# Optimization experiments

Measured on AMD Instinct MI355X. Metric: run time of the kernel, lower is better.

## Reference

```python
import jax, jax.numpy as jnp
import numpy as np

N = 50000   # total nodes
E = 600000  # total edges
D = 128     # feature dim (node_dim == all gcn_dims)
G = 128     # graphs in batch
LN_EPS = 1e-5


def setup_inputs() -> dict:
    key = jax.random.key(0)
    ks = jax.random.split(key, 16)
    inp = {
        "x": jax.random.normal(ks[0], (N, D), dtype=jnp.float32),
        "edge_index": jax.random.randint(ks[1], (2, E), 0, N),
        "batch": jnp.sort(jax.random.randint(ks[2], (N,), 0, G)),
    }
    for l in range(3):
        inp[f"W{l}"] = jax.random.normal(ks[3 + 4 * l], (D, D), dtype=jnp.float32) / np.float32(np.sqrt(D))
        inp[f"b{l}"] = jnp.zeros((D,), jnp.float32)
        inp[f"g{l}"] = jnp.ones((D,), jnp.float32)   # LayerNorm weight
        inp[f"be{l}"] = jnp.zeros((D,), jnp.float32)  # LayerNorm bias
    return inp


def _gcn_norm(edge_index):
    # PyG GCNConv default: add self-loops, symmetric deg^-1/2 normalization.
    loop = jnp.arange(N, dtype=edge_index.dtype)
    src = jnp.concatenate([edge_index[0], loop])
    dst = jnp.concatenate([edge_index[1], loop])
    deg = jax.ops.segment_sum(jnp.ones(src.shape[0], jnp.float32), dst, num_segments=N)
    dinv = jnp.where(deg > 0, jax.lax.rsqrt(deg), 0.0)
    norm = dinv[src] * dinv[dst]  # [E+N]
    return src, dst, norm


def _block(x, src, dst, norm, W, b, g, be):
    # GCNConv: gather-transform-scatter
    h = x @ W                                   # [N, D]
    msg = h[src] * norm[:, None]                # [E+N, D] gather + scale
    out = jax.ops.segment_sum(msg, dst, num_segments=N) + b
    # LayerNorm
    mu = jnp.mean(out, axis=-1, keepdims=True)
    var = jnp.mean((out - mu) ** 2, axis=-1, keepdims=True)
    out = (out - mu) * jax.lax.rsqrt(var + LN_EPS) * g + be
    # residual (Identity since in==out channels) + SiLU
    return jax.nn.silu(out + x)


def reference(x, edge_index, batch, W0, b0, g0, be0, W1, b1, g1, be1, W2, b2, g2, be2):
    src, dst, norm = _gcn_norm(edge_index)
    params = [(W0, b0, g0, be0), (W1, b1, g1, be1), (W2, b2, g2, be2)]
    for (W, b, g, be) in params:
        x = _block(x, src, dst, norm, W, b, g, be)
    # global mean pool over batch ids
    counts = jax.ops.segment_sum(jnp.ones((N,), jnp.float32), batch, num_segments=G)
    sums = jax.ops.segment_sum(x, batch, num_segments=G)
    return sums / jnp.maximum(counts, 1.0)[:, None]
```

## Files before the change

### kernel.cpp

```cpp
#include <hip/hip_runtime.h>
#include <math.h>

#define DD 128

typedef __attribute__((ext_vector_type(8))) short short8;
typedef __attribute__((ext_vector_type(4))) float f32x4;

__device__ __forceinline__ unsigned short f2b(float f) {
    unsigned int x = __float_as_uint(f);
    return (unsigned short)((x + 0x7FFFu + ((x >> 16) & 1u)) >> 16);
}
__device__ __forceinline__ float b2f(unsigned short u) {
    return __uint_as_float(((unsigned int)u) << 16);
}

__global__ __launch_bounds__(256) void k_count(const int* __restrict__ dst, int* __restrict__ cnt, int E) {
    int e = blockIdx.x * 256 + threadIdx.x;
    if (e < E) atomicAdd(&cnt[dst[e]], 1);
}

__global__ __launch_bounds__(256) void k_scan1(const int* __restrict__ cnt, int* __restrict__ part, int N) {
    __shared__ int lds[256];
    int t = threadIdx.x;
    int i = blockIdx.x * 256 + t;
    lds[t] = (i < N) ? cnt[i] : 0;
    __syncthreads();
#pragma unroll
    for (int off = 128; off > 0; off >>= 1) {
        if (t < off) lds[t] += lds[t + off];
        __syncthreads();
    }
    if (t == 0) part[blockIdx.x] = lds[0];
}

__global__ __launch_bounds__(1024) void k_scan2(int* __restrict__ part, int* __restrict__ rowptr,
                                                int nblk, int N) {
    __shared__ int lds[1024];
    int t = threadIdx.x;
    int v = (t < nblk) ? part[t] : 0;
    lds[t] = v;
    __syncthreads();
    for (int off = 1; off < 1024; off <<= 1) {
        int u = (t >= off) ? lds[t - off] : 0;
        __syncthreads();
        lds[t] += u;
        __syncthreads();
    }
    if (t < nblk) part[t] = lds[t] - v;
    if (t == 1023) rowptr[N] = lds[1023];
}

__global__ __launch_bounds__(256) void k_scan3(const int* __restrict__ cnt, const int* __restrict__ part,
                                               int* __restrict__ rowptr, float* __restrict__ dinv, int N) {
    __shared__ int lds[256];
    int t = threadIdx.x;
    int i = blockIdx.x * 256 + t;
    int v = (i < N) ? cnt[i] : 0;
    lds[t] = v;
    __syncthreads();
    for (int off = 1; off < 256; off <<= 1) {
        int u = (t >= off) ? lds[t - off] : 0;
        __syncthreads();
        lds[t] += u;
        __syncthreads();
    }
    if (i < N) {
        rowptr[i] = part[blockIdx.x] + lds[t] - v;
        dinv[i] = rsqrtf((float)v + 1.0f);
    }
}

__global__ __launch_bounds__(256) void k_fill(const int* __restrict__ src, const int* __restrict__ dst,
                                              const float* __restrict__ dinv, const int* __restrict__ rowptr,
                                              int* __restrict__ cursor, int2* __restrict__ adj, int E) {
    int e = blockIdx.x * 256 + threadIdx.x;
    if (e >= E) return;
    int s = src[e], d = dst[e];
    int pos = atomicAdd(&cursor[d], 1);
    float w = dinv[s] * dinv[d];
    adj[rowptr[d] + pos] = make_int2(s, __float_as_int(w));
}

__global__ __launch_bounds__(256) void k_prepW3(const float* __restrict__ W0, const float* __restrict__ W1,
                                                const float* __restrict__ W2, unsigned short* __restrict__ T0,
                                                unsigned short* __restrict__ T1, unsigned short* __restrict__ T2) {
    int l = blockIdx.x >> 6;
    const float* W = (l == 0) ? W0 : (l == 1) ? W1 : W2;
    unsigned short* WT = (l == 0) ? T0 : (l == 1) ? T1 : T2;
    int idx = (blockIdx.x & 63) * 256 + threadIdx.x;
    int k = idx >> 7, c = idx & 127;
    WT[c * DD + k] = f2b(W[idx]);
}

template <int IN_BF16>
__global__ __launch_bounds__(256) void k_gemm_mfma(const void* __restrict__ Xv,
                                                   const unsigned short* __restrict__ WT,
                                                   unsigned short* __restrict__ H, int N) {
    __shared__ __align__(16) unsigned short sB[DD * DD];
    __shared__ __align__(16) unsigned short sA[64 * DD];
    int tid = threadIdx.x;
    long row0 = (long)blockIdx.x * 64;

#pragma unroll
    for (int i = 0; i < 8; ++i) {
        int q = tid + 256 * i;
        int c = q >> 4, j = q & 15;
        short8 v = *(const short8*)(WT + q * 8);
        int byte = c * 256 + ((j * 16) ^ ((c & 7) << 4));
        *(short8*)((char*)sB + byte) = v;
    }
#pragma unroll
    for (int i = 0; i < 4; ++i) {
        int q = tid + 256 * i;
        int r = q >> 4, j = q & 15;
        short8 v;
        if (IN_BF16) {
#pragma unroll
            for (int z = 0; z < 8; ++z) v[z] = 0;
            if (row0 + r < N) v = *(const short8*)((const unsigned short*)Xv + (row0 + r) * DD + j * 8);
        } else {
            float4 a0 = make_float4(0.f, 0.f, 0.f, 0.f), a1 = a0;
            if (row0 + r < N) {
                const float4* p = (const float4*)((const float*)Xv + (row0 + r) * DD + j * 8);
                a0 = p[0];
                a1 = p[1];
            }
            v[0] = (short)f2b(a0.x); v[1] = (short)f2b(a0.y);
            v[2] = (short)f2b(a0.z); v[3] = (short)f2b(a0.w);
            v[4] = (short)f2b(a1.x); v[5] = (short)f2b(a1.y);
            v[6] = (short)f2b(a1.z); v[7] = (short)f2b(a1.w);
        }
        int byte = r * 256 + ((j * 16) ^ ((r & 7) << 4));
        *(short8*)((char*)sA + byte) = v;
    }
    __syncthreads();

    int w = tid >> 6, l = tid & 63;
    int lr = l & 15, kg = l >> 4;
    f32x4 acc[8] = {};

#pragma unroll
    for (int step = 0; step < 4; ++step) {
        int ar = w * 16 + lr;
        int abyte = ar * 256 + ((step * 64 + kg * 16) ^ ((ar & 7) << 4));
        short8 af = *(const short8*)((const char*)sA + abyte);
#pragma unroll
        for (int ct = 0; ct < 8; ++ct) {
            int c = ct * 16 + lr;
            int bbyte = c * 256 + ((step * 64 + kg * 16) ^ ((c & 7) << 4));
            short8 bf = *(const short8*)((const char*)sB + bbyte);
            acc[ct] = __builtin_amdgcn_mfma_f32_16x16x32_bf16(af, bf, acc[ct], 0, 0, 0);
        }
    }

#pragma unroll
    for (int ct = 0; ct < 8; ++ct) {
#pragma unroll
        for (int reg = 0; reg < 4; ++reg) {
            long r = row0 + w * 16 + kg * 4 + reg;
            if (r < N) H[r * DD + ct * 16 + lr] = f2b(acc[ct][reg]);
        }
    }
}

template <int IN_BF16>
__global__ __launch_bounds__(256) void k_agg(const unsigned short* __restrict__ h, const void* __restrict__ xin,
                                             const int* __restrict__ rowptr, const int2* __restrict__ adj,
                                             const float* __restrict__ dinv, const float* __restrict__ b,
                                             const float* __restrict__ g, const float* __restrict__ be,
                                             unsigned int* __restrict__ xout, int N) {
    int row = blockIdx.x * 4 + (threadIdx.x >> 6);
    if (row >= N) return;
    int lane = threadIdx.x & 63;
    const unsigned int* hu = (const unsigned int*)h;

    float dv = dinv[row];
    float dv2 = dv * dv;
    unsigned int us = hu[(size_t)row * 64 + lane];
    float2 bv = ((const float2*)b)[lane];
    float2 acc = make_float2(fmaf(b2f((unsigned short)(us & 0xFFFF)), dv2, bv.x),
                             fmaf(b2f((unsigned short)(us >> 16)), dv2, bv.y));

    int beg = rowptr[row], end = rowptr[row + 1];
    for (int j0 = beg; j0 < end; j0 += 64) {
        int myj = j0 + lane;
        int2 a = make_int2(0, 0);
        if (myj < end) a = adj[myj];
        int cnt = min(64, end - j0);
        int cntR = (cnt + 7) & ~7;
        for (int k0 = 0; k0 < cntR; k0 += 8) {
            unsigned int un[8];
            float wt[8];
#pragma unroll
            for (int u = 0; u < 8; ++u) {
                int s = __shfl(a.x, k0 + u, 64);
                wt[u] = __int_as_float(__shfl(a.y, k0 + u, 64));
                un[u] = hu[(size_t)s * 64 + lane];
            }
#pragma unroll
            for (int u = 0; u < 8; ++u) {
                acc.x = fmaf(wt[u], b2f((unsigned short)(un[u] & 0xFFFF)), acc.x);
                acc.y = fmaf(wt[u], b2f((unsigned short)(un[u] >> 16)), acc.y);
            }
        }
    }

    float ssum = acc.x + acc.y;
#pragma unroll
    for (int o = 32; o > 0; o >>= 1) ssum += __shfl_xor(ssum, o, 64);
    float mu = ssum * (1.0f / 128.0f);
    float dx0 = acc.x - mu, dx1 = acc.y - mu;
    float vs = dx0 * dx0 + dx1 * dx1;
#pragma unroll
    for (int o = 32; o > 0; o >>= 1) vs += __shfl_xor(vs, o, 64);
    float rstd = rsqrtf(vs * (1.0f / 128.0f) + 1e-5f);

    float2 gv = ((const float2*)g)[lane];
    float2 bev = ((const float2*)be)[lane];
    float2 xv;
    if (IN_BF16) {
        unsigned int xu = ((const unsigned int*)xin)[(size_t)row * 64 + lane];
        xv = make_float2(b2f((unsigned short)(xu & 0xFFFF)), b2f((unsigned short)(xu >> 16)));
    } else {
        xv = ((const float2*)xin)[(size_t)row * 64 + lane];
    }
    float a0 = fmaf(dx0 * rstd, gv.x, bev.x) + xv.x;
    float a1 = fmaf(dx1 * rstd, gv.y, bev.y) + xv.y;
    a0 = a0 / (1.0f + expf(-a0));
    a1 = a1 / (1.0f + expf(-a1));
    xout[(size_t)row * 64 + lane] = ((unsigned int)f2b(a1) << 16) | (unsigned int)f2b(a0);
}

__global__ __launch_bounds__(256) void k_pool2(const unsigned int* __restrict__ x, const int* __restrict__ batch,
                                               float* __restrict__ out, int N) {
    int gi = blockIdx.x;
    int lo = 0, hi = N;
    while (lo < hi) { int m = (lo + hi) >> 1; if (batch[m] < gi) lo = m + 1; else hi = m; }
    int beg = lo;
    lo = beg; hi = N;
    while (lo < hi) { int m = (lo + hi) >> 1; if (batch[m] < gi + 1) lo = m + 1; else hi = m; }
    int end = lo;

    int tid = threadIdx.x;
    int wave = tid >> 6, lane = tid & 63;
    float2 acc = make_float2(0.f, 0.f);
    for (int r = beg + wave; r < end; r += 4) {
        unsigned int u = x[(size_t)r * 64 + lane];
        acc.x += b2f((unsigned short)(u & 0xFFFF));
        acc.y += b2f((unsigned short)(u >> 16));
    }
    __shared__ float part[4][DD];
    ((float2*)part[wave])[lane] = acc;
    __syncthreads();
    if (wave == 0) {
        float sx = 0.f, sy = 0.f;
#pragma unroll
        for (int w = 0; w < 4; ++w) {
            float2 v = ((const float2*)part[w])[lane];
            sx += v.x;
            sy += v.y;
        }
        float inv = 1.0f / fmaxf((float)(end - beg), 1.0f);
        ((float2*)(out + (size_t)gi * DD))[lane] = make_float2(sx * inv, sy * inv);
    }
}

extern "C" void kernel_launch(void* const* d_in, const int* in_sizes, int n_in,
                              void* d_out, int out_size, void* d_ws, size_t ws_size,
                              hipStream_t stream) {
    const float* x = (const float*)d_in[0];
    const int* edge = (const int*)d_in[1];
    const int* batch = (const int*)d_in[2];
    const float* W[3] = {(const float*)d_in[3], (const float*)d_in[7], (const float*)d_in[11]};
    const float* b[3] = {(const float*)d_in[4], (const float*)d_in[8], (const float*)d_in[12]};
    const float* g[3] = {(const float*)d_in[5], (const float*)d_in[9], (const float*)d_in[13]};
    const float* be[3] = {(const float*)d_in[6], (const float*)d_in[10], (const float*)d_in[14]};

    int N = in_sizes[0] / DD;
    int E = in_sizes[1] / 2;
    int G = out_size / DD;
    const int* srcI = edge;
    const int* dstI = edge + E;

    int nblk = (N + 255) / 256;

    char* ws = (char*)d_ws;
    size_t ND = (size_t)N * DD;
    unsigned int* bufX = (unsigned int*)ws;           ws += ND * 2;
    unsigned short* bufH = (unsigned short*)ws;       ws += ND * 2;
    unsigned short* wt[3];
    for (int l = 0; l < 3; ++l) { wt[l] = (unsigned short*)ws; ws += (size_t)DD * DD * 2; }
    float* dinv = (float*)ws;                         ws += (size_t)N * 4;
    int* cnt = (int*)ws;                              ws += (size_t)N * 4;
    int* cursor = (int*)ws;                           ws += (size_t)N * 4;
    int* rowptr = (int*)ws;                           ws += (size_t)(N + 1) * 4;
    int* part = (int*)ws;                             ws += (size_t)nblk * 4;
    ws = (char*)(((uintptr_t)ws + 15) & ~(uintptr_t)15);
    int2* adj = (int2*)ws;

    hipMemsetAsync(cnt, 0, (size_t)N * 2 * 4, stream);

    k_count<<<(E + 255) / 256, 256, 0, stream>>>(dstI, cnt, E);
    k_scan1<<<nblk, 256, 0, stream>>>(cnt, part, N);
    k_scan2<<<1, 1024, 0, stream>>>(part, rowptr, nblk, N);
    k_scan3<<<nblk, 256, 0, stream>>>(cnt, part, rowptr, dinv, N);
    k_fill<<<(E + 255) / 256, 256, 0, stream>>>(srcI, dstI, dinv, rowptr, cursor, adj, E);
    k_prepW3<<<192, 256, 0, stream>>>(W[0], W[1], W[2], wt[0], wt[1], wt[2]);

    int gblk = (N + 63) / 64, ablk = (N + 3) / 4;
    k_gemm_mfma<0><<<gblk, 256, 0, stream>>>(x, wt[0], bufH, N);
    k_agg<0><<<ablk, 256, 0, stream>>>(bufH, x, rowptr, adj, dinv, b[0], g[0], be[0], bufX, N);
    for (int l = 1; l < 3; ++l) {
        k_gemm_mfma<1><<<gblk, 256, 0, stream>>>(bufX, wt[l], bufH, N);
        k_agg<1><<<ablk, 256, 0, stream>>>(bufH, bufX, rowptr, adj, dinv, b[l], g[l], be[l], bufX, N);
    }

    k_pool2<<<G, 256, 0, stream>>>(bufX, batch, (float*)d_out, N);
}
```

Before: 240.8 us.

## Fuse setup kernels, double GEMM row tile, deepen aggregation gather batch

After: 238.8 us. About the same (-0.8%).

```diff
diff --git a/kernel.cpp b/kernel.cpp
--- a/kernel.cpp
+++ b/kernel.cpp
@@ -14,9 +14,22 @@
     return __uint_as_float(((unsigned int)u) << 16);
 }
 
-__global__ __launch_bounds__(256) void k_count(const int* __restrict__ dst, int* __restrict__ cnt, int E) {
-    int e = blockIdx.x * 256 + threadIdx.x;
-    if (e < E) atomicAdd(&cnt[dst[e]], 1);
+__global__ __launch_bounds__(256) void k_setup(const int* __restrict__ dst, int* __restrict__ cnt, int E,
+                                               const float* __restrict__ W0, const float* __restrict__ W1,
+                                               const float* __restrict__ W2, unsigned short* __restrict__ T0,
+                                               unsigned short* __restrict__ T1, unsigned short* __restrict__ T2) {
+    int bid = blockIdx.x;
+    if (bid < 192) {
+        int l = bid >> 6;
+        const float* W = (l == 0) ? W0 : (l == 1) ? W1 : W2;
+        unsigned short* WT = (l == 0) ? T0 : (l == 1) ? T1 : T2;
+        int idx = (bid & 63) * 256 + threadIdx.x;
+        int k = idx >> 7, c = idx & 127;
+        WT[c * DD + k] = f2b(W[idx]);
+    } else {
+        int e = (bid - 192) * 256 + threadIdx.x;
+        if (e < E) atomicAdd(&cnt[dst[e]], 1);
+    }
 }
 
 __global__ __launch_bounds__(256) void k_scan1(const int* __restrict__ cnt, int* __restrict__ part, int N) {
@@ -81,25 +94,14 @@
     adj[rowptr[d] + pos] = make_int2(s, __float_as_int(w));
 }
 
-__global__ __launch_bounds__(256) void k_prepW3(const float* __restrict__ W0, const float* __restrict__ W1,
-                                                const float* __restrict__ W2, unsigned short* __restrict__ T0,
-                                                unsigned short* __restrict__ T1, unsigned short* __restrict__ T2) {
-    int l = blockIdx.x >> 6;
-    const float* W = (l == 0) ? W0 : (l == 1) ? W1 : W2;
-    unsigned short* WT = (l == 0) ? T0 : (l == 1) ? T1 : T2;
-    int idx = (blockIdx.x & 63) * 256 + threadIdx.x;
-    int k = idx >> 7, c = idx & 127;
-    WT[c * DD + k] = f2b(W[idx]);
-}
-
 template <int IN_BF16>
 __global__ __launch_bounds__(256) void k_gemm_mfma(const void* __restrict__ Xv,
                                                    const unsigned short* __restrict__ WT,
                                                    unsigned short* __restrict__ H, int N) {
     __shared__ __align__(16) unsigned short sB[DD * DD];
-    __shared__ __align__(16) unsigned short sA[64 * DD];
+    __shared__ __align__(16) unsigned short sA[DD * DD];
     int tid = threadIdx.x;
-    long row0 = (long)blockIdx.x * 64;
+    long row0 = (long)blockIdx.x * 128;
 
 #pragma unroll
     for (int i = 0; i < 8; ++i) {
@@ -110,7 +112,7 @@
         *(short8*)((char*)sB + byte) = v;
     }
 #pragma unroll
-    for (int i = 0; i < 4; ++i) {
+    for (int i = 0; i < 8; ++i) {
         int q = tid + 256 * i;
         int r = q >> 4, j = q & 15;
         short8 v;
@@ -137,19 +139,20 @@
 
     int w = tid >> 6, l = tid & 63;
     int lr = l & 15, kg = l >> 4;
-    f32x4 acc[8] = {};
+    int ar0 = w * 32 + lr, ar1 = w * 32 + 16 + lr;
+    f32x4 acc0[8] = {}, acc1[8] = {};
 
 #pragma unroll
     for (int step = 0; step < 4; ++step) {
-        int ar = w * 16 + lr;
-        int abyte = ar * 256 + ((step * 64 + kg * 16) ^ ((ar & 7) << 4));
-        short8 af = *(const short8*)((const char*)sA + abyte);
+        int koff = step * 64 + kg * 16;
+        short8 a0 = *(const short8*)((const char*)sA + ar0 * 256 + (koff ^ ((ar0 & 7) << 4)));
+        short8 a1 = *(const short8*)((const char*)sA + ar1 * 256 + (koff ^ ((ar1 & 7) << 4)));
 #pragma unroll
         for (int ct = 0; ct < 8; ++ct) {
             int c = ct * 16 + lr;
-            int bbyte = c * 256 + ((step * 64 + kg * 16) ^ ((c & 7) << 4));
-            short8 bf = *(const short8*)((const char*)sB + bbyte);
-            acc[ct] = __builtin_amdgcn_mfma_f32_16x16x32_bf16(af, bf, acc[ct], 0, 0, 0);
+            short8 bf = *(const short8*)((const char*)sB + c * 256 + (koff ^ ((c & 7) << 4)));
+            acc0[ct] = __builtin_amdgcn_mfma_f32_16x16x32_bf16(a0, bf, acc0[ct], 0, 0, 0);
+            acc1[ct] = __builtin_amdgcn_mfma_f32_16x16x32_bf16(a1, bf, acc1[ct], 0, 0, 0);
         }
     }
 
@@ -157,8 +160,10 @@
     for (int ct = 0; ct < 8; ++ct) {
 #pragma unroll
         for (int reg = 0; reg < 4; ++reg) {
-            long r = row0 + w * 16 + kg * 4 + reg;
-            if (r < N) H[r * DD + ct * 16 + lr] = f2b(acc[ct][reg]);
+            long r = row0 + w * 32 + kg * 4 + reg;
+            if (r < N) H[r * DD + ct * 16 + lr] = f2b(acc0[ct][reg]);
+            long r2 = r + 16;
+            if (r2 < N) H[r2 * DD + ct * 16 + lr] = f2b(acc1[ct][reg]);
         }
     }
 }
@@ -187,18 +192,18 @@
         int2 a = make_int2(0, 0);
         if (myj < end) a = adj[myj];
         int cnt = min(64, end - j0);
-        int cntR = (cnt + 7) & ~7;
-        for (int k0 = 0; k0 < cntR; k0 += 8) {
-            unsigned int un[8];
-            float wt[8];
-#pragma unroll
-            for (int u = 0; u < 8; ++u) {
+        int cntR = (cnt + 15) & ~15;
+        for (int k0 = 0; k0 < cntR; k0 += 16) {
+            unsigned int un[16];
+            float wt[16];
+#pragma unroll
+            for (int u = 0; u < 16; ++u) {
                 int s = __shfl(a.x, k0 + u, 64);
                 wt[u] = __int_as_float(__shfl(a.y, k0 + u, 64));
                 un[u] = hu[(size_t)s * 64 + lane];
             }
 #pragma unroll
-            for (int u = 0; u < 8; ++u) {
+            for (int u = 0; u < 16; ++u) {
                 acc.x = fmaf(wt[u], b2f((unsigned short)(un[u] & 0xFFFF)), acc.x);
                 acc.y = fmaf(wt[u], b2f((unsigned short)(un[u] >> 16)), acc.y);
             }
@@ -300,14 +305,13 @@
 
     hipMemsetAsync(cnt, 0, (size_t)N * 2 * 4, stream);
 
-    k_count<<<(E + 255) / 256, 256, 0, stream>>>(dstI, cnt, E);
+    k_setup<<<192 + (E + 255) / 256, 256, 0, stream>>>(dstI, cnt, E, W[0], W[1], W[2], wt[0], wt[1], wt[2]);
     k_scan1<<<nblk, 256, 0, stream>>>(cnt, part, N);
     k_scan2<<<1, 1024, 0, stream>>>(part, rowptr, nblk, N);
     k_scan3<<<nblk, 256, 0, stream>>>(cnt, part, rowptr, dinv, N);
     k_fill<<<(E + 255) / 256, 256, 0, stream>>>(srcI, dstI, dinv, rowptr, cursor, adj, E);
-    k_prepW3<<<192, 256, 0, stream>>>(W[0], W[1], W[2], wt[0], wt[1], wt[2]);
-
-    int gblk = (N + 63) / 64, ablk = (N + 3) / 4;
+
+    int gblk = (N + 127) / 128, ablk = (N + 3) / 4;
     k_gemm_mfma<0><<<gblk, 256, 0, stream>>>(x, wt[0], bufH, N);
     k_agg<0><<<ablk, 256, 0, stream>>>(bufH, x, rowptr, adj, dinv, b[0], g[0], be[0], bufX, N);
     for (int l = 1; l < 3; ++l) {
```
